# Performance work log

Measured on AMD Instinct MI355X. Metric: run time of the kernel, lower is better.

The kernel has to match this reference:

```python
import jax, jax.numpy as jnp
import numpy as np

H = 256
L = 2048
OPINION_LIST = jnp.array([19, 20, 21, 33, 34, 35, 41, 42, 43, 44, 45, 46])


def setup_inputs() -> dict:
    key = jax.random.key(0)
    ks = jax.random.split(key, 8)
    B = 8
    opinion_features = jax.random.normal(ks[0], (B, L, H), dtype=jnp.float32)
    text_features = jax.random.normal(ks[1], (B, L, H), dtype=jnp.float32)
    pos_ids = jax.random.randint(ks[2], (B, L), 0, 47)
    scale = 1.0 / np.sqrt(H)
    Wt = jax.random.normal(ks[3], (H, H), dtype=jnp.float32) * scale
    bt = jax.random.normal(ks[4], (H,), dtype=jnp.float32) * scale
    Wo = jax.random.normal(ks[5], (H, H), dtype=jnp.float32) * scale
    wa = jax.random.normal(ks[6], (2 * H,), dtype=jnp.float32) * scale
    ba = jax.random.normal(ks[7], (1,), dtype=jnp.float32) * scale
    return {"opinion_features": opinion_features, "text_features": text_features,
            "pos_ids": pos_ids, "Wt": Wt, "bt": bt, "Wo": Wo, "wa": wa, "ba": ba}


def position_bias(pos_ids):
    # base: 0.5 on diagonal, 1/log2(2+|i-j|) elsewhere  -> (L, L)
    idx = jnp.arange(L)
    dist = jnp.abs(idx[:, None] - idx[None, :]).astype(jnp.float32)
    base = jnp.where(dist == 0, 0.5, 1.0 / jnp.log2(2.0 + dist))
    # per-token column multiplier: 8 if POS tag is an opinion tag else 1 -> (B, L)
    is_op = (pos_ids[..., None] == OPINION_LIST).any(-1)
    mult = jnp.where(is_op, 8.0, 1.0).astype(jnp.float32)
    return base[None, :, :] * mult[:, None, :]  # (B, L, L)


def reference(opinion_features, text_features, pos_ids, Wt, bt, Wo, wa, ba):
    pos_m = position_bias(pos_ids)                      # (B, L, L)
    t = text_features @ Wt.T + bt                       # (B, L, H)
    o = opinion_features @ Wo.T                         # (B, L, H)
    # tanh(concat([t_i, o_j])) @ wa + ba decomposes additively since tanh is elementwise
    st = jnp.tanh(t) @ wa[:H]                           # (B, L)
    so = jnp.tanh(o) @ wa[H:]                           # (B, L)
    scores = (st[:, :, None] + so[:, None, :] + ba[0]) * pos_m  # (B, L, L)
    att = jax.nn.softmax(scores, axis=-1)
    return att @ opinion_features                       # (B, L, H)
```

## Files before the change

kernel.cpp:

```cpp
#include <hip/hip_runtime.h>

#define B_ 8
#define L_ 2048
#define H_ 256

typedef _Float16 half8 __attribute__((ext_vector_type(8)));
typedef _Float16 half4_t __attribute__((ext_vector_type(4)));
typedef float f32x4 __attribute__((ext_vector_type(4)));

__device__ __forceinline__ float fast_tanh(float x) {
    const float e2 = __expf(2.f * x);
    return 1.f - 2.f * __builtin_amdgcn_rcpf(e2 + 1.f);
}

#define PHASE_BARRIER() do {                                   \
        asm volatile("s_waitcnt lgkmcnt(0)" ::: "memory");     \
        __builtin_amdgcn_s_barrier();                          \
        __builtin_amdgcn_sched_barrier(0);                     \
    } while (0)

__global__ __launch_bounds__(256, 2) void prep_kernel(
    const float* __restrict__ opin, const float* __restrict__ text,
    const int* __restrict__ pos_ids,
    const float* __restrict__ Wt, const float* __restrict__ bt,
    const float* __restrict__ Wo, const float* __restrict__ wa,
    const float* __restrict__ ba,
    float* __restrict__ ws_st, float2* __restrict__ ws_cm,
    _Float16* __restrict__ vtg)
{
    __shared__ __align__(16) _Float16 a_lds[4][8][512];
    __shared__ __align__(16) _Float16 w_lds[2][16][512];

    const int tid  = threadIdx.x;
    const int lane = tid & 63;
    const int rg   = tid >> 6;
    const int mat  = blockIdx.x & 1;
    const size_t g0 = (size_t)(blockIdx.x >> 1) * 64;

    const float* __restrict__ src = mat ? opin : text;
    const float* __restrict__ W   = mat ? Wo   : Wt;

    f32x4 wregA[8], wregB[8];
#define ISSUE_W(DST, KC) do {                                                   \
        _Pragma("unroll")                                                       \
        for (int p = 0; p < 8; ++p) {                                           \
            const float* p_ = W + (p * 32 + (tid >> 3)) * 256 + (KC) * 32 +     \
                              (tid & 7) * 4;                                    \
            asm volatile("global_load_dwordx4 %0, %1, off"                      \
                         : "=v"(DST[p]) : "v"(p_));                             \
        }                                                                       \
    } while (0)

    ISSUE_W(wregA, 0);

    for (int v = 0; v < 16; ++v) {
        const int idx = v * 256 + tid;
        const int row = idx >> 6;
        const int k   = (idx & 63) * 4;
        const float4 f = *(const float4*)(src + (g0 + row) * 256 + k);
        half4_t h = { (_Float16)f.x, (_Float16)f.y, (_Float16)f.z, (_Float16)f.w };
        const int off = ((row & 15) + 16 * ((k >> 3) & 3)) * 8 + (k & 7);
        *(half4_t*)&a_lds[row >> 4][k >> 5][off] = h;
    }
    PHASE_BARRIER();

    f32x4 acc[16];
#pragma unroll
    for (int nt = 0; nt < 16; ++nt) acc[nt] = (f32x4){0.f, 0.f, 0.f, 0.f};

    auto wbody = [&](const int kc, f32x4 (&cur)[8], f32x4 (&nxt)[8]) {
        asm volatile("s_waitcnt vmcnt(0)" ::: "memory");
        __builtin_amdgcn_sched_barrier(0);
        if (kc < 7) ISSUE_W(nxt, kc + 1);
#pragma unroll
        for (int p = 0; p < 8; ++p) {
            const int n = p * 32 + (tid >> 3);
            const int k = (tid & 7) * 4;
            const float4 f = __builtin_bit_cast(float4, cur[p]);
            half4_t h = { (_Float16)f.x, (_Float16)f.y, (_Float16)f.z, (_Float16)f.w };
            const int off = ((n & 15) + 16 * (k >> 3)) * 8 + (k & 7);
            *(half4_t*)&w_lds[kc & 1][n >> 4][off] = h;
        }
        PHASE_BARRIER();
        const half8 afrag = *(const half8*)&a_lds[rg][kc][lane * 8];
#pragma unroll
        for (int nt = 0; nt < 16; ++nt) {
            const half8 bfrag = *(const half8*)&w_lds[kc & 1][nt][lane * 8];
            acc[nt] = __builtin_amdgcn_mfma_f32_16x16x32_f16(afrag, bfrag, acc[nt], 0, 0, 0);
        }
    };
    for (int kc = 0; kc < 8; kc += 2) {
        wbody(kc,     wregA, wregB);
        wbody(kc + 1, wregB, wregA);
    }
#undef ISSUE_W

    const int em = lane & 15, q = lane >> 4;
    float rowsum[4] = {0.f, 0.f, 0.f, 0.f};
#pragma unroll
    for (int nt = 0; nt < 16; ++nt) {
        const int col  = nt * 16 + em;
        const float btv = mat ? 0.f : bt[col];
        const float wav = wa[mat * 256 + col];
#pragma unroll
        for (int r = 0; r < 4; ++r)
            rowsum[r] += fast_tanh(acc[nt][r] + btv) * wav;
    }
#pragma unroll
    for (int r = 0; r < 4; ++r) {
        float s = rowsum[r];
        s += __shfl_xor(s, 1, 64);
        s += __shfl_xor(s, 2, 64);
        s += __shfl_xor(s, 4, 64);
        s += __shfl_xor(s, 8, 64);
        if (em == 0) {
            const size_t grow = g0 + rg * 16 + q * 4 + r;
            if (mat == 0) {
                ws_st[grow] = s;
            } else {
                const int p = pos_ids[grow];
                const bool isop = (p==19)|(p==20)|(p==21)|(p==33)|(p==34)|(p==35)|((p>=41)&(p<=46));
                const float mult = isop ? 8.f : 1.f;
                const float c = s + ba[0];
                ws_cm[grow] = make_float2(c * mult, mult);
            }
        }
    }

    if (mat == 1) {
        const int h = tid;
        const size_t b = g0 >> 11;
        const int kcj = (int)((g0 & 2047) >> 6);
        const int kc = h >> 5, kq = (h >> 3) & 3, jh = h & 7;
        _Float16 vals[64];
#pragma unroll
        for (int r = 0; r < 64; ++r)
            vals[r] = a_lds[r >> 4][kc][((r & 15) + 16 * kq) * 8 + jh];
        _Float16* dst = vtg + ((size_t)b * 32 + kcj) * 16384 + h * 8;
#pragma unroll
        for (int w = 0; w < 8; ++w)
            *(half8*)(dst + w * 2048) = *(half8*)&vals[w * 8];
    }
}

__global__ __launch_bounds__(256, 2) void attn_kernel(
    const float* __restrict__ ws_st, const float2* __restrict__ ws_cm,
    const _Float16* __restrict__ vtg, float* __restrict__ out)
{
    __shared__ float t_lds[2048];
    __shared__ float cm_lds[4096];
    __shared__ __align__(16) _Float16 p_lds[2][2][2][512];
    __shared__ __align__(16) float alpha_lds[2][32];
    __shared__ float z_lds[32];

    const int tid  = threadIdx.x;
    const int lane = tid & 63;
    const int hq   = tid >> 6;
    const int em   = lane & 15;
    const int q4   = lane >> 4;

    const int b  = blockIdx.x & 7;
    const int i0 = (blockIdx.x >> 3) * 32;

    const int row = tid >> 3;
    const int jg  = tid & 7;
    const int gi  = i0 + row;

    const _Float16* __restrict__ vb =
        vtg + ((size_t)b * 32) * 16384 + q4 * 2048 + (hq * 64 + em) * 8;

    f32x4 vbA[2][4], vbB[2][4];
#define ISSUE_VB(DST, KC) do {                                                  \
        const _Float16* p_ = vb + (size_t)((KC) & 31) * 16384;                  \
        _Pragma("unroll")                                                       \
        for (int ks = 0; ks < 2; ++ks)                                          \
        _Pragma("unroll")                                                       \
        for (int ht = 0; ht < 4; ++ht)                                          \
            asm volatile("global_load_dwordx4 %0, %1, off"                      \
                         : "=v"(DST[ks][ht]) : "v"(p_ + ks * 8192 + ht * 128)); \
    } while (0)

    ISSUE_VB(vbA, 0);

#pragma unroll
    for (int v = 0; v < 8; ++v) {
        const int d = tid * 8 + v;
        const float bv = (d == 0) ? 0.5f : 1.0f / __log2f(2.f + (float)d);
        t_lds[d] = bv * 1.44269504088896f;
    }
#pragma unroll
    for (int v = 0; v < 4; ++v) {
        const int idx = (v * 256 + tid) * 4;
        *(float4*)&cm_lds[idx] =
            *(const float4*)((const float*)(ws_cm + b * 2048) + idx);
    }

    const float sti = ws_st[b * 2048 + gi];

    f32x4 acc[2][4];
#pragma unroll
    for (int rt = 0; rt < 2; ++rt)
#pragma unroll
        for (int ht = 0; ht < 4; ++ht) acc[rt][ht] = (f32x4){0.f, 0.f, 0.f, 0.f};
    float m_run = -1e30f;
    float zacc  = 0.f;

    PHASE_BARRIER();

    auto scores = [&](const int kc, const int nbuf) {
        const int j0 = kc * 64;
        float s_arr[8];
        float mx = -1e30f;
        const float* __restrict__ cmp = &cm_lds[(j0 + jg * 8) * 2];
#pragma unroll
        for (int w = 0; w < 4; ++w) {
            const float4 c4 = *(const float4*)(cmp + w * 4);
            const int jj = j0 + jg * 8 + w * 2;
            int d0 = gi - jj;     d0 = d0 < 0 ? -d0 : d0;
            int d1 = gi - jj - 1; d1 = d1 < 0 ? -d1 : d1;
            const float s0 = (sti * c4.y + c4.x) * t_lds[d0];
            const float s1 = (sti * c4.w + c4.z) * t_lds[d1];
            s_arr[2 * w]     = s0;
            s_arr[2 * w + 1] = s1;
            mx = fmaxf(mx, fmaxf(s0, s1));
        }
        mx = fmaxf(mx, __shfl_xor(mx, 1, 64));
        mx = fmaxf(mx, __shfl_xor(mx, 2, 64));
        mx = fmaxf(mx, __shfl_xor(mx, 4, 64));

        const float m_new = fmaxf(m_run, mx);
        const float alpha = __builtin_amdgcn_exp2f(m_run - m_new);
        float zl = 0.f;
        half8 pv;
#pragma unroll
        for (int v = 0; v < 8; ++v) {
            const float p = __builtin_amdgcn_exp2f(s_arr[v] - m_new);
            zl += p;
            pv[v] = (_Float16)p;
        }
        zacc  = zacc * alpha + zl;
        m_run = m_new;

        const int kq = jg & 3;
        const int slot = (((row & 15) ^ (kq << 1)) + 16 * kq);
        *(half8*)&p_lds[nbuf][row >> 4][jg >> 2][slot * 8] = pv;
        if (jg == 0) alpha_lds[nbuf][row] = alpha;
    };

    auto rescale = [&](const int cbuf) {
        const float4 a0 = *(const float4*)&alpha_lds[cbuf][q4 * 4];
        const float4 a1 = *(const float4*)&alpha_lds[cbuf][16 + q4 * 4];
        const float ar[2][4] = {{a0.x, a0.y, a0.z, a0.w}, {a1.x, a1.y, a1.z, a1.w}};
        bool upd = false;
#pragma unroll
        for (int rt = 0; rt < 2; ++rt)
#pragma unroll
            for (int r = 0; r < 4; ++r) upd |= (ar[rt][r] != 1.f);
        if (__any(upd)) {
#pragma unroll
            for (int rt = 0; rt < 2; ++rt)
#pragma unroll
                for (int ht = 0; ht < 4; ++ht)
#pragma unroll
                    for (int r = 0; r < 4; ++r)
                        acc[rt][ht][r] *= ar[rt][r];
        }
    };

    auto mfma_step = [&](const int cbuf, f32x4 (&vbuf)[2][4]) {
        const int sl8 = ((em ^ (q4 << 1)) + 16 * q4) * 8;
#pragma unroll
        for (int ks = 0; ks < 2; ++ks) {
            const half8 a0 = *(const half8*)&p_lds[cbuf][0][ks][sl8];
            const half8 a1 = *(const half8*)&p_lds[cbuf][1][ks][sl8];
#pragma unroll
            for (int ht = 0; ht < 4; ++ht) {
                const half8 bh = __builtin_bit_cast(half8, vbuf[ks][ht]);
                acc[0][ht] = __builtin_amdgcn_mfma_f32_16x16x32_f16(a0, bh, acc[0][ht], 0, 0, 0);
                acc[1][ht] = __builtin_amdgcn_mfma_f32_16x16x32_f16(a1, bh, acc[1][ht], 0, 0, 0);
            }
        }
    };

    scores(0, 0);
    PHASE_BARRIER();

    for (int kc = 0; kc < 32; kc += 2) {
        ISSUE_VB(vbB, kc + 1);
        rescale(0);
        asm volatile("s_waitcnt vmcnt(8)" ::: "memory");
        __builtin_amdgcn_sched_barrier(0);
        mfma_step(0, vbA);
        scores(kc + 1, 1);
        PHASE_BARRIER();

        ISSUE_VB(vbA, kc + 2);
        rescale(1);
        asm volatile("s_waitcnt vmcnt(8)" ::: "memory");
        __builtin_amdgcn_sched_barrier(0);
        mfma_step(1, vbB);
        if (kc + 2 < 32) scores(kc + 2, 0);
        PHASE_BARRIER();
    }
#undef ISSUE_VB

    zacc += __shfl_xor(zacc, 1, 64);
    zacc += __shfl_xor(zacc, 2, 64);
    zacc += __shfl_xor(zacc, 4, 64);
    if (jg == 0) z_lds[row] = zacc;
    __syncthreads();

#pragma unroll
    for (int rt = 0; rt < 2; ++rt) {
#pragma unroll
        for (int r = 0; r < 4; ++r) {
            const int orow = rt * 16 + q4 * 4 + r;
            const float rz = 1.f / z_lds[orow];
#pragma unroll
            for (int ht = 0; ht < 4; ++ht)
                out[((size_t)b * 2048 + i0 + orow) * 256 + hq * 64 + ht * 16 + em] =
                    acc[rt][ht][r] * rz;
        }
    }
}

extern "C" void kernel_launch(void* const* d_in, const int* in_sizes, int n_in,
                              void* d_out, int out_size, void* d_ws, size_t ws_size,
                              hipStream_t stream) {
    const float* opin  = (const float*)d_in[0];
    const float* text  = (const float*)d_in[1];
    const int* pos_ids = (const int*)d_in[2];
    const float* Wt    = (const float*)d_in[3];
    const float* bt    = (const float*)d_in[4];
    const float* Wo    = (const float*)d_in[5];
    const float* wa    = (const float*)d_in[6];
    const float* ba    = (const float*)d_in[7];
    float* out         = (float*)d_out;

    float*  ws_st = (float*)d_ws;
    float2* ws_cm = (float2*)((char*)d_ws + 65536);
    _Float16* vtg = (_Float16*)((char*)d_ws + 65536 + 131072);

    prep_kernel<<<512, 256, 0, stream>>>(opin, text, pos_ids, Wt, bt, Wo, wa, ba,
                                         ws_st, ws_cm, vtg);
    attn_kernel<<<512, 256, 0, stream>>>(ws_st, ws_cm, vtg, out);
}
```

Before: 139.6 us.

## Split attention K-chunk across two wave groups with 512-thread blocks

Doubles the attn_kernel block to 512 threads. The two halves of the waves each handle one 32-wide k-slice of every 64-key chunk for the MFMA, and the score computation is spread over 16 lanes per row instead of 8. Partial accumulators from the second half are reduced through a new padded LDS buffer before the output write. The aim is more waves in flight to hide V-load and softmax latency. The costs are about 33KB of extra LDS, which may limit blocks per CU, and an extra cross-wave reduction at the end.

New measurement: 138.9 us. About the same (-0.5%).

```diff
diff --git a/kernel.cpp b/kernel.cpp
--- a/kernel.cpp
+++ b/kernel.cpp
@@ -143,7 +143,7 @@
     }
 }
 
-__global__ __launch_bounds__(256, 2) void attn_kernel(
+__global__ __launch_bounds__(512, 4) void attn_kernel(
     const float* __restrict__ ws_st, const float2* __restrict__ ws_cm,
     const _Float16* __restrict__ vtg, float* __restrict__ out)
 {
@@ -152,45 +152,46 @@
     __shared__ __align__(16) _Float16 p_lds[2][2][2][512];
     __shared__ __align__(16) float alpha_lds[2][32];
     __shared__ float z_lds[32];
+    __shared__ float red_lds[32][260];
 
     const int tid  = threadIdx.x;
     const int lane = tid & 63;
-    const int hq   = tid >> 6;
+    const int wid  = tid >> 6;
+    const int hq   = wid & 3;
+    const int kh   = wid >> 2;
     const int em   = lane & 15;
     const int q4   = lane >> 4;
 
     const int b  = blockIdx.x & 7;
     const int i0 = (blockIdx.x >> 3) * 32;
 
-    const int row = tid >> 3;
-    const int jg  = tid & 7;
+    const int row = tid >> 4;
+    const int jg  = tid & 15;
     const int gi  = i0 + row;
 
     const _Float16* __restrict__ vb =
-        vtg + ((size_t)b * 32) * 16384 + q4 * 2048 + (hq * 64 + em) * 8;
-
-    f32x4 vbA[2][4], vbB[2][4];
+        vtg + (size_t)b * 524288 + kh * 8192 + q4 * 2048 + (hq * 64 + em) * 8;
+
+    f32x4 vbA[4], vbB[4];
 #define ISSUE_VB(DST, KC) do {                                                  \
         const _Float16* p_ = vb + (size_t)((KC) & 31) * 16384;                  \
         _Pragma("unroll")                                                       \
-        for (int ks = 0; ks < 2; ++ks)                                          \
-        _Pragma("unroll")                                                       \
         for (int ht = 0; ht < 4; ++ht)                                          \
             asm volatile("global_load_dwordx4 %0, %1, off"                      \
-                         : "=v"(DST[ks][ht]) : "v"(p_ + ks * 8192 + ht * 128)); \
+                         : "=v"(DST[ht]) : "v"(p_ + ht * 128));                 \
     } while (0)
 
     ISSUE_VB(vbA, 0);
 
 #pragma unroll
-    for (int v = 0; v < 8; ++v) {
-        const int d = tid * 8 + v;
+    for (int v = 0; v < 4; ++v) {
+        const int d = tid * 4 + v;
         const float bv = (d == 0) ? 0.5f : 1.0f / __log2f(2.f + (float)d);
         t_lds[d] = bv * 1.44269504088896f;
     }
 #pragma unroll
-    for (int v = 0; v < 4; ++v) {
-        const int idx = (v * 256 + tid) * 4;
+    for (int v = 0; v < 2; ++v) {
+        const int idx = (v * 512 + tid) * 4;
         *(float4*)&cm_lds[idx] =
             *(const float4*)((const float*)(ws_cm + b * 2048) + idx);
     }
@@ -209,31 +210,34 @@
 
     auto scores = [&](const int kc, const int nbuf) {
         const int j0 = kc * 64;
-        float s_arr[8];
+        float s_arr[4];
         float mx = -1e30f;
-        const float* __restrict__ cmp = &cm_lds[(j0 + jg * 8) * 2];
-#pragma unroll
-        for (int w = 0; w < 4; ++w) {
-            const float4 c4 = *(const float4*)(cmp + w * 4);
-            const int jj = j0 + jg * 8 + w * 2;
+        const float* __restrict__ cmp = &cm_lds[(j0 + jg * 4) * 2];
+        const float4 ca = *(const float4*)(cmp + 0);
+        const float4 cb = *(const float4*)(cmp + 4);
+        {
+            const int jj = j0 + jg * 4;
             int d0 = gi - jj;     d0 = d0 < 0 ? -d0 : d0;
             int d1 = gi - jj - 1; d1 = d1 < 0 ? -d1 : d1;
-            const float s0 = (sti * c4.y + c4.x) * t_lds[d0];
-            const float s1 = (sti * c4.w + c4.z) * t_lds[d1];
-            s_arr[2 * w]     = s0;
-            s_arr[2 * w + 1] = s1;
-            mx = fmaxf(mx, fmaxf(s0, s1));
+            int d2 = gi - jj - 2; d2 = d2 < 0 ? -d2 : d2;
+            int d3 = gi - jj - 3; d3 = d3 < 0 ? -d3 : d3;
+            s_arr[0] = (sti * ca.y + ca.x) * t_lds[d0];
+            s_arr[1] = (sti * ca.w + ca.z) * t_lds[d1];
+            s_arr[2] = (sti * cb.y + cb.x) * t_lds[d2];
+            s_arr[3] = (sti * cb.w + cb.z) * t_lds[d3];
+            mx = fmaxf(fmaxf(s_arr[0], s_arr[1]), fmaxf(s_arr[2], s_arr[3]));
         }
         mx = fmaxf(mx, __shfl_xor(mx, 1, 64));
         mx = fmaxf(mx, __shfl_xor(mx, 2, 64));
         mx = fmaxf(mx, __shfl_xor(mx, 4, 64));
+        mx = fmaxf(mx, __shfl_xor(mx, 8, 64));
 
         const float m_new = fmaxf(m_run, mx);
         const float alpha = __builtin_amdgcn_exp2f(m_run - m_new);
         float zl = 0.f;
-        half8 pv;
-#pragma unroll
-        for (int v = 0; v < 8; ++v) {
+        half4_t pv;
+#pragma unroll
+        for (int v = 0; v < 4; ++v) {
             const float p = __builtin_amdgcn_exp2f(s_arr[v] - m_new);
             zl += p;
             pv[v] = (_Float16)p;
@@ -241,9 +245,13 @@
         zacc  = zacc * alpha + zl;
         m_run = m_new;
 
-        const int kq = jg & 3;
-        const int slot = (((row & 15) ^ (kq << 1)) + 16 * kq);
-        *(half8*)&p_lds[nbuf][row >> 4][jg >> 2][slot * 8] = pv;
+        {
+            const int mrow = row & 15;
+            const int ks = jg >> 3;
+            const int kq = (jg & 7) >> 1;
+            const int slot = ((mrow ^ (kq << 1)) + 16 * kq);
+            *(half4_t*)&p_lds[nbuf][row >> 4][ks][slot * 8 + (jg & 1) * 4] = pv;
+        }
         if (jg == 0) alpha_lds[nbuf][row] = alpha;
     };
 
@@ -267,18 +275,15 @@
         }
     };
 
-    auto mfma_step = [&](const int cbuf, f32x4 (&vbuf)[2][4]) {
+    auto mfma_step = [&](const int cbuf, f32x4 (&vbuf)[4]) {
         const int sl8 = ((em ^ (q4 << 1)) + 16 * q4) * 8;
-#pragma unroll
-        for (int ks = 0; ks < 2; ++ks) {
-            const half8 a0 = *(const half8*)&p_lds[cbuf][0][ks][sl8];
-            const half8 a1 = *(const half8*)&p_lds[cbuf][1][ks][sl8];
-#pragma unroll
-            for (int ht = 0; ht < 4; ++ht) {
-                const half8 bh = __builtin_bit_cast(half8, vbuf[ks][ht]);
-                acc[0][ht] = __builtin_amdgcn_mfma_f32_16x16x32_f16(a0, bh, acc[0][ht], 0, 0, 0);
-                acc[1][ht] = __builtin_amdgcn_mfma_f32_16x16x32_f16(a1, bh, acc[1][ht], 0, 0, 0);
-            }
+        const half8 a0 = *(const half8*)&p_lds[cbuf][0][kh][sl8];
+        const half8 a1 = *(const half8*)&p_lds[cbuf][1][kh][sl8];
+#pragma unroll
+        for (int ht = 0; ht < 4; ++ht) {
+            const half8 bh = __builtin_bit_cast(half8, vbuf[ht]);
+            acc[0][ht] = __builtin_amdgcn_mfma_f32_16x16x32_f16(a0, bh, acc[0][ht], 0, 0, 0);
+            acc[1][ht] = __builtin_amdgcn_mfma_f32_16x16x32_f16(a1, bh, acc[1][ht], 0, 0, 0);
         }
     };
 
@@ -288,7 +293,7 @@
     for (int kc = 0; kc < 32; kc += 2) {
         ISSUE_VB(vbB, kc + 1);
         rescale(0);
-        asm volatile("s_waitcnt vmcnt(8)" ::: "memory");
+        asm volatile("s_waitcnt vmcnt(4)" ::: "memory");
         __builtin_amdgcn_sched_barrier(0);
         mfma_step(0, vbA);
         scores(kc + 1, 1);
@@ -296,7 +301,7 @@
 
         ISSUE_VB(vbA, kc + 2);
         rescale(1);
-        asm volatile("s_waitcnt vmcnt(8)" ::: "memory");
+        asm volatile("s_waitcnt vmcnt(4)" ::: "memory");
         __builtin_amdgcn_sched_barrier(0);
         mfma_step(1, vbB);
         if (kc + 2 < 32) scores(kc + 2, 0);
@@ -307,19 +312,33 @@
     zacc += __shfl_xor(zacc, 1, 64);
     zacc += __shfl_xor(zacc, 2, 64);
     zacc += __shfl_xor(zacc, 4, 64);
+    zacc += __shfl_xor(zacc, 8, 64);
     if (jg == 0) z_lds[row] = zacc;
+
+    if (kh == 1) {
+#pragma unroll
+        for (int rt = 0; rt < 2; ++rt)
+#pragma unroll
+            for (int ht = 0; ht < 4; ++ht)
+#pragma unroll
+                for (int r = 0; r < 4; ++r)
+                    red_lds[rt * 16 + q4 * 4 + r][hq * 64 + ht * 16 + em] = acc[rt][ht][r];
+    }
     __syncthreads();
 
-#pragma unroll
-    for (int rt = 0; rt < 2; ++rt) {
-#pragma unroll
-        for (int r = 0; r < 4; ++r) {
-            const int orow = rt * 16 + q4 * 4 + r;
-            const float rz = 1.f / z_lds[orow];
-#pragma unroll
-            for (int ht = 0; ht < 4; ++ht)
-                out[((size_t)b * 2048 + i0 + orow) * 256 + hq * 64 + ht * 16 + em] =
-                    acc[rt][ht][r] * rz;
+    if (kh == 0) {
+#pragma unroll
+        for (int rt = 0; rt < 2; ++rt) {
+#pragma unroll
+            for (int r = 0; r < 4; ++r) {
+                const int orow = rt * 16 + q4 * 4 + r;
+                const float rz = 1.f / z_lds[orow];
+#pragma unroll
+                for (int ht = 0; ht < 4; ++ht) {
+                    const float v = acc[rt][ht][r] + red_lds[orow][hq * 64 + ht * 16 + em];
+                    out[((size_t)b * 2048 + i0 + orow) * 256 + hq * 64 + ht * 16 + em] = v * rz;
+                }
+            }
         }
     }
 }
@@ -343,5 +362,5 @@
 
     prep_kernel<<<512, 256, 0, stream>>>(opin, text, pos_ids, Wt, bt, Wo, wa, ba,
                                          ws_st, ws_cm, vtg);
-    attn_kernel<<<512, 256, 0, stream>>>(ws_st, ws_cm, vtg, out);
+    attn_kernel<<<512, 512, 0, stream>>>(ws_st, ws_cm, vtg, out);
 }
```
